# Optimization experiments

Measured on AMD Instinct MI355X. Metric: run time of the kernel, lower is better.

Reference implementation:

```python
import jax, jax.numpy as jnp
import numpy as np

B, S, D = 16, 4096, 128
LN_EPS = 1e-5
REC_EPS = 1e-8


def setup_inputs() -> dict:
    key = jax.random.key(0)
    k1, k2, k3, k4 = jax.random.split(key, 4)
    return {
        "C": jax.random.normal(k1, (B, S, D), dtype=jnp.float32),
        "V": jax.random.normal(k2, (B, S, D), dtype=jnp.float32),
        "W": jax.random.normal(k3, (B, S, D), dtype=jnp.float32),
        "encoder_context": jax.random.normal(k4, (B, D), dtype=jnp.float32),
        "time_modulation": jnp.full((1, 1, D), 0.5, dtype=jnp.float32),
        "context_modulation": jnp.full((1, D), 0.5, dtype=jnp.float32),
        "ln_weight": jnp.ones((D,), dtype=jnp.float32),
        "ln_bias": jnp.zeros((D,), dtype=jnp.float32),
    }


def reference(C, V, W, encoder_context, time_modulation, context_modulation, ln_weight, ln_bias):
    b_, s_, d_ = C.shape
    tm = time_modulation[0, 0]  # [D]
    # context gate is time-invariant: compute once
    ctx_add = jax.nn.sigmoid(encoder_context * context_modulation) * encoder_context  # [B,D]

    def step(carry, xs):
        a, bst = carry  # a: [B,1], bst: [B,D]
        c_t, v_t, w_t = xs  # each [B,D]
        decay = jax.nn.sigmoid(w_t * tm)  # [B,D]
        ec = jnp.exp(c_t)  # [B,D]
        a = decay.mean(axis=1, keepdims=True) * a + ec.sum(axis=1, keepdims=True)
        bst = decay * bst + ec * v_t + ctx_add
        out_t = bst / (a + REC_EPS)
        return (a, bst), out_t

    a0 = jnp.zeros((b_, 1), dtype=C.dtype)
    b0 = jnp.zeros((b_, d_), dtype=C.dtype)
    xs = (jnp.swapaxes(C, 0, 1), jnp.swapaxes(V, 0, 1), jnp.swapaxes(W, 0, 1))  # [S,B,D]
    _, ys = jax.lax.scan(step, (a0, b0), xs)  # ys: [S,B,D]
    res = jnp.swapaxes(ys, 0, 1)  # [B,S,D]

    mu = jnp.mean(res, axis=-1, keepdims=True)
    var = jnp.var(res, axis=-1, keepdims=True)
    normed = (res - mu) * jax.lax.rsqrt(var + LN_EPS)
    return normed * ln_weight + ln_bias
```

## Files before the change

kernel.cpp:

```cpp
#include <hip/hip_runtime.h>

#define BB   16
#define SS   4096
#define DD   128
#define NCH  256
#define TT   (SS / NCH)
#define GPB  4
#define NTHR 128

#define DT   16
#define SUBS 16
#define CPS  (NCH / SUBS)

#define LN_EPS  1e-5f
#define REC_EPS 1e-8f

__device__ __forceinline__ float fast_rcp(float x) { return __builtin_amdgcn_rcpf(x); }
__device__ __forceinline__ float sigm(float x) { return fast_rcp(1.0f + __expf(-x)); }

__device__ __forceinline__ unsigned pack_de(float d, float e) {
    unsigned ud = (__float_as_uint(d) + 0x8000u) >> 16;
    unsigned ue = (__float_as_uint(e) + 0x8000u) & 0xFFFF0000u;
    return ue | ud;
}
__device__ __forceinline__ float de_lo(unsigned u) { return __uint_as_float(u << 16); }
__device__ __forceinline__ float de_hi(unsigned u) { return __uint_as_float(u & 0xFFFF0000u); }

__device__ __forceinline__ void red2(float& a, float& b) {
#pragma unroll
    for (int m = 16; m >= 1; m >>= 1) {
        a += __shfl_xor(a, m, 64);
        b += __shfl_xor(b, m, 64);
    }
}

__global__ __launch_bounds__(NTHR) void pass1_kernel(
    const float* __restrict__ C, const float* __restrict__ V, const float* __restrict__ W,
    const float* __restrict__ enc, const float* __restrict__ tmod, const float* __restrict__ cmod,
    unsigned* __restrict__ DE,
    float* __restrict__ Pbuf, float* __restrict__ Qbuf,
    float* __restrict__ PaBuf, float* __restrict__ QaBuf,
    float* __restrict__ mbuf, float* __restrict__ ebuf)
{
    const int grp  = threadIdx.x >> 5;
    const int lane = threadIdx.x & 31;
    const int gc   = blockIdx.x * GPB + grp;
    const int b    = gc >> 8;
    const int ch   = gc & (NCH - 1);
    const int d4   = lane << 2;

    const float4 tm = *(const float4*)(tmod + d4);
    const float4 cm = *(const float4*)(cmod + d4);
    const float4 ec = *(const float4*)(enc + b * DD + d4);
    float4 ctx;
    ctx.x = sigm(ec.x * cm.x) * ec.x;
    ctx.y = sigm(ec.y * cm.y) * ec.y;
    ctx.z = sigm(ec.z * cm.z) * ec.z;
    ctx.w = sigm(ec.w * cm.w) * ec.w;

    float4 P = make_float4(1.f, 1.f, 1.f, 1.f);
    float4 Q = make_float4(0.f, 0.f, 0.f, 0.f);
    float pa = 1.f, qa = 0.f;

    const int t0 = ch * TT;
    const size_t base = ((size_t)b * SS + t0) * DD + d4;
    const float4* Cp = (const float4*)(C + base);
    const float4* Vp = (const float4*)(V + base);
    const float4* Wp = (const float4*)(W + base);
    uint4* DEp = (uint4*)(DE + base);

#pragma unroll 4
    for (int t = 0; t < TT; ++t) {
        const float4 c4 = Cp[t * (DD / 4)];
        const float4 v4 = Vp[t * (DD / 4)];
        const float4 w4 = Wp[t * (DD / 4)];
        float4 dec, e4;
        dec.x = sigm(w4.x * tm.x); dec.y = sigm(w4.y * tm.y);
        dec.z = sigm(w4.z * tm.z); dec.w = sigm(w4.w * tm.w);
        e4.x = __expf(c4.x); e4.y = __expf(c4.y);
        e4.z = __expf(c4.z); e4.w = __expf(c4.w);

        uint4 u;
        u.x = pack_de(dec.x, e4.x); u.y = pack_de(dec.y, e4.y);
        u.z = pack_de(dec.z, e4.z); u.w = pack_de(dec.w, e4.w);
        DEp[t * (DD / 4)] = u;

        Q.x = dec.x * Q.x + (e4.x * v4.x + ctx.x);
        Q.y = dec.y * Q.y + (e4.y * v4.y + ctx.y);
        Q.z = dec.z * Q.z + (e4.z * v4.z + ctx.z);
        Q.w = dec.w * Q.w + (e4.w * v4.w + ctx.w);
        P.x *= dec.x; P.y *= dec.y; P.z *= dec.z; P.w *= dec.w;

        float sd = (dec.x + dec.y) + (dec.z + dec.w);
        float se = (e4.x + e4.y) + (e4.z + e4.w);
        red2(sd, se);
        const float mt = sd * (1.0f / DD);
        pa *= mt;
        qa = mt * qa + se;
        if (lane == 0) {
            mbuf[(size_t)b * SS + t0 + t] = mt;
            ebuf[(size_t)b * SS + t0 + t] = se;
        }
    }

    *(float4*)(Pbuf + (size_t)gc * DD + d4) = P;
    *(float4*)(Qbuf + (size_t)gc * DD + d4) = Q;
    if (lane == 0) { PaBuf[gc] = pa; QaBuf[gc] = qa; }
}

__global__ __launch_bounds__(256) void pass2_kernel(
    const float* __restrict__ Pbuf, const float* __restrict__ Qbuf,
    const float* __restrict__ PaBuf, const float* __restrict__ QaBuf,
    float* __restrict__ bst0, float* __restrict__ a0)
{
    const int b   = blockIdx.x >> 3;
    const int dt  = blockIdx.x & 7;
    const int tid = threadIdx.x;
    const int dl  = tid & (DT - 1);
    const int sub = tid >> 4;
    const int d   = dt * DT + dl;

    __shared__ float cP[SUBS][DT], cQ[SUBS][DT], ent[SUBS][DT];
    __shared__ float sPa[NCH], sQa[NCH];

    const int ch0 = sub * CPS;
    const size_t base = ((size_t)b * NCH + ch0) * DD + d;
    float Pr[CPS], Qr[CPS];
    float p = 1.f, q = 0.f;
#pragma unroll
    for (int i = 0; i < CPS; ++i) {
        Pr[i] = Pbuf[base + (size_t)i * DD];
        Qr[i] = Qbuf[base + (size_t)i * DD];
        q = Pr[i] * q + Qr[i];
        p = Pr[i] * p;
    }
    cP[sub][dl] = p; cQ[sub][dl] = q;
    __syncthreads();

    if (tid < DT) {
        float s = 0.f;
#pragma unroll
        for (int sb = 0; sb < SUBS; ++sb) {
            ent[sb][tid] = s;
            s = cP[sb][tid] * s + cQ[sb][tid];
        }
    }
    __syncthreads();

    float s = ent[sub][dl];
#pragma unroll
    for (int i = 0; i < CPS; ++i) {
        bst0[base + (size_t)i * DD] = s;
        s = Pr[i] * s + Qr[i];
    }

    if (dt == 0) {
        float pa = PaBuf[b * NCH + tid];
        float qa = QaBuf[b * NCH + tid];
#pragma unroll
        for (int off = 1; off < NCH; off <<= 1) {
            sPa[tid] = pa; sQa[tid] = qa;
            __syncthreads();
            if (tid >= off) {
                const float pp = sPa[tid - off], qq = sQa[tid - off];
                qa = pa * qq + qa;
                pa = pa * pp;
            }
            __syncthreads();
        }
        sQa[tid] = qa;
        __syncthreads();
        a0[b * NCH + tid] = (tid == 0) ? 0.f : sQa[tid - 1];
    }
}

__global__ __launch_bounds__(NTHR) void pass3_kernel(
    const float* __restrict__ V, const unsigned* __restrict__ DE,
    const float* __restrict__ enc, const float* __restrict__ cmod,
    const float* __restrict__ lnw, const float* __restrict__ lnb,
    const float* __restrict__ bst0, const float* __restrict__ a0,
    const float* __restrict__ mbuf, const float* __restrict__ ebuf,
    float* __restrict__ out)
{
    const int grp  = threadIdx.x >> 5;
    const int lane = threadIdx.x & 31;
    const int gc   = blockIdx.x * GPB + grp;
    const int b    = gc >> 8;
    const int ch   = gc & (NCH - 1);
    const int d4   = lane << 2;

    const float4 cm = *(const float4*)(cmod + d4);
    const float4 ec = *(const float4*)(enc + b * DD + d4);
    float4 ctx;
    ctx.x = sigm(ec.x * cm.x) * ec.x;
    ctx.y = sigm(ec.y * cm.y) * ec.y;
    ctx.z = sigm(ec.z * cm.z) * ec.z;
    ctx.w = sigm(ec.w * cm.w) * ec.w;
    const float4 gw = *(const float4*)(lnw + d4);
    const float4 gb = *(const float4*)(lnb + d4);

    float4 bst = *(const float4*)(bst0 + (size_t)gc * DD + d4);
    float a = a0[gc];

    const int t0 = ch * TT;
    const size_t base = ((size_t)b * SS + t0) * DD + d4;
    const float4* Vp = (const float4*)(V + base);
    const uint4*  DEp = (const uint4*)(DE + base);
    float4* Op = (float4*)(out + base);
    const float* mp = mbuf + (size_t)b * SS + t0;
    const float* ep = ebuf + (size_t)b * SS + t0;

#pragma unroll 4
    for (int t = 0; t < TT; ++t) {
        const float4 v4 = Vp[t * (DD / 4)];
        const uint4  u  = DEp[t * (DD / 4)];
        const float mt = mp[t];
        const float et = ep[t];

        a = mt * a + et;
        bst.x = de_lo(u.x) * bst.x + (de_hi(u.x) * v4.x + ctx.x);
        bst.y = de_lo(u.y) * bst.y + (de_hi(u.y) * v4.y + ctx.y);
        bst.z = de_lo(u.z) * bst.z + (de_hi(u.z) * v4.z + ctx.z);
        bst.w = de_lo(u.w) * bst.w + (de_hi(u.w) * v4.w + ctx.w);

        const float inva = fast_rcp(a + REC_EPS);
        float4 o;
        o.x = bst.x * inva; o.y = bst.y * inva;
        o.z = bst.z * inva; o.w = bst.w * inva;

        float s1 = (o.x + o.y) + (o.z + o.w);
        float s2 = (o.x * o.x + o.y * o.y) + (o.z * o.z + o.w * o.w);
        red2(s1, s2);
        const float mu  = s1 * (1.0f / DD);
        const float var = s2 * (1.0f / DD) - mu * mu;
        const float rs  = rsqrtf(var + LN_EPS);

        float4 r;
        r.x = (o.x - mu) * rs * gw.x + gb.x;
        r.y = (o.y - mu) * rs * gw.y + gb.y;
        r.z = (o.z - mu) * rs * gw.z + gb.z;
        r.w = (o.w - mu) * rs * gw.w + gb.w;
        Op[t * (DD / 4)] = r;
    }
}

extern "C" void kernel_launch(void* const* d_in, const int* in_sizes, int n_in,
                              void* d_out, int out_size, void* d_ws, size_t ws_size,
                              hipStream_t stream)
{
    const float* C    = (const float*)d_in[0];
    const float* V    = (const float*)d_in[1];
    const float* W    = (const float*)d_in[2];
    const float* enc  = (const float*)d_in[3];
    const float* tmod = (const float*)d_in[4];
    const float* cmod = (const float*)d_in[5];
    const float* lnw  = (const float*)d_in[6];
    const float* lnb  = (const float*)d_in[7];
    float* out = (float*)d_out;

    float* ws    = (float*)d_ws;
    unsigned* DEbuf = (unsigned*)ws;
    float* Pbuf  = ws    + (size_t)BB * SS * DD;
    float* Qbuf  = Pbuf  + (size_t)BB * NCH * DD;
    float* bst0  = Qbuf  + (size_t)BB * NCH * DD;
    float* mbuf  = bst0  + (size_t)BB * NCH * DD;
    float* ebuf  = mbuf  + (size_t)BB * SS;
    float* PaBuf = ebuf  + (size_t)BB * SS;
    float* QaBuf = PaBuf + (size_t)BB * NCH;
    float* a0Buf = QaBuf + (size_t)BB * NCH;

    const int nblk = BB * NCH / GPB;
    pass1_kernel<<<nblk, NTHR, 0, stream>>>(C, V, W, enc, tmod, cmod, DEbuf,
                                            Pbuf, Qbuf, PaBuf, QaBuf, mbuf, ebuf);
    pass2_kernel<<<BB * 8, 256, 0, stream>>>(Pbuf, Qbuf, PaBuf, QaBuf, bst0, a0Buf);
    pass3_kernel<<<nblk, NTHR, 0, stream>>>(V, DEbuf, enc, cmod, lnw, lnb,
                                            bst0, a0Buf, mbuf, ebuf, out);
}
```

Measured before the change: 162.7 us.

## Map each chunk to a full 64-lane wave with DPP reductions

Pass 1 and pass 3 now give each sequential chunk a full 64-lane wavefront, with each lane handling two channels (float2) instead of four. Previously a chunk used 32 lanes handling float4. The cross-lane sums now use DPP row shifts plus a readlane instead of shfl_xor butterflies, and the per-step decay-mean and exp-sum scalars are merged into one float2 buffer. This doubles thread count and per-lane parallelism across the latency-bound recurrence and aims to cut reduction cost. In exchange, memory accesses become narrower 8-byte loads.

```diff
diff --git a/kernel.cpp b/kernel.cpp
--- a/kernel.cpp
+++ b/kernel.cpp
@@ -5,8 +5,8 @@
 #define DD   128
 #define NCH  256
 #define TT   (SS / NCH)
-#define GPB  4
-#define NTHR 128
+#define WPB  4
+#define NTHR 256
 
 #define DT   16
 #define SUBS 16
@@ -26,85 +26,84 @@
 __device__ __forceinline__ float de_lo(unsigned u) { return __uint_as_float(u << 16); }
 __device__ __forceinline__ float de_hi(unsigned u) { return __uint_as_float(u & 0xFFFF0000u); }
 
-__device__ __forceinline__ void red2(float& a, float& b) {
-#pragma unroll
-    for (int m = 16; m >= 1; m >>= 1) {
-        a += __shfl_xor(a, m, 64);
-        b += __shfl_xor(b, m, 64);
-    }
-}
-
-__global__ __launch_bounds__(NTHR) void pass1_kernel(
+template<int CTRL>
+__device__ __forceinline__ float dpp_mov0(float x) {
+    return __int_as_float(
+        __builtin_amdgcn_update_dpp(0, __float_as_int(x), CTRL, 0xF, 0xF, true));
+}
+
+__device__ __forceinline__ void wave_red2(float& a, float& b) {
+    a += dpp_mov0<0x111>(a); b += dpp_mov0<0x111>(b);
+    a += dpp_mov0<0x112>(a); b += dpp_mov0<0x112>(b);
+    a += dpp_mov0<0x114>(a); b += dpp_mov0<0x114>(b);
+    a += dpp_mov0<0x118>(a); b += dpp_mov0<0x118>(b);
+    a += dpp_mov0<0x142>(a); b += dpp_mov0<0x142>(b);
+    a += dpp_mov0<0x143>(a); b += dpp_mov0<0x143>(b);
+    a = __int_as_float(__builtin_amdgcn_readlane(__float_as_int(a), 63));
+    b = __int_as_float(__builtin_amdgcn_readlane(__float_as_int(b), 63));
+}
+
+__global__ __launch_bounds__(NTHR, 4) void pass1_kernel(
     const float* __restrict__ C, const float* __restrict__ V, const float* __restrict__ W,
     const float* __restrict__ enc, const float* __restrict__ tmod, const float* __restrict__ cmod,
     unsigned* __restrict__ DE,
     float* __restrict__ Pbuf, float* __restrict__ Qbuf,
     float* __restrict__ PaBuf, float* __restrict__ QaBuf,
-    float* __restrict__ mbuf, float* __restrict__ ebuf)
-{
-    const int grp  = threadIdx.x >> 5;
-    const int lane = threadIdx.x & 31;
-    const int gc   = blockIdx.x * GPB + grp;
+    float2* __restrict__ MEbuf)
+{
+    const int wv   = threadIdx.x >> 6;
+    const int lane = threadIdx.x & 63;
+    const int gc   = blockIdx.x * WPB + wv;
     const int b    = gc >> 8;
     const int ch   = gc & (NCH - 1);
-    const int d4   = lane << 2;
-
-    const float4 tm = *(const float4*)(tmod + d4);
-    const float4 cm = *(const float4*)(cmod + d4);
-    const float4 ec = *(const float4*)(enc + b * DD + d4);
-    float4 ctx;
+    const int d2   = lane << 1;
+
+    const float2 tm = *(const float2*)(tmod + d2);
+    const float2 cm = *(const float2*)(cmod + d2);
+    const float2 ec = *(const float2*)(enc + b * DD + d2);
+    float2 ctx;
     ctx.x = sigm(ec.x * cm.x) * ec.x;
     ctx.y = sigm(ec.y * cm.y) * ec.y;
-    ctx.z = sigm(ec.z * cm.z) * ec.z;
-    ctx.w = sigm(ec.w * cm.w) * ec.w;
-
-    float4 P = make_float4(1.f, 1.f, 1.f, 1.f);
-    float4 Q = make_float4(0.f, 0.f, 0.f, 0.f);
+
+    float2 P = make_float2(1.f, 1.f);
+    float2 Q = make_float2(0.f, 0.f);
     float pa = 1.f, qa = 0.f;
 
     const int t0 = ch * TT;
-    const size_t base = ((size_t)b * SS + t0) * DD + d4;
-    const float4* Cp = (const float4*)(C + base);
-    const float4* Vp = (const float4*)(V + base);
-    const float4* Wp = (const float4*)(W + base);
-    uint4* DEp = (uint4*)(DE + base);
+    const size_t base = ((size_t)b * SS + t0) * DD + d2;
+    const float2* Cp = (const float2*)(C + base);
+    const float2* Vp = (const float2*)(V + base);
+    const float2* Wp = (const float2*)(W + base);
+    uint2* DEp = (uint2*)(DE + base);
 
 #pragma unroll 4
     for (int t = 0; t < TT; ++t) {
-        const float4 c4 = Cp[t * (DD / 4)];
-        const float4 v4 = Vp[t * (DD / 4)];
-        const float4 w4 = Wp[t * (DD / 4)];
-        float4 dec, e4;
-        dec.x = sigm(w4.x * tm.x); dec.y = sigm(w4.y * tm.y);
-        dec.z = sigm(w4.z * tm.z); dec.w = sigm(w4.w * tm.w);
-        e4.x = __expf(c4.x); e4.y = __expf(c4.y);
-        e4.z = __expf(c4.z); e4.w = __expf(c4.w);
-
-        uint4 u;
-        u.x = pack_de(dec.x, e4.x); u.y = pack_de(dec.y, e4.y);
-        u.z = pack_de(dec.z, e4.z); u.w = pack_de(dec.w, e4.w);
-        DEp[t * (DD / 4)] = u;
-
-        Q.x = dec.x * Q.x + (e4.x * v4.x + ctx.x);
-        Q.y = dec.y * Q.y + (e4.y * v4.y + ctx.y);
-        Q.z = dec.z * Q.z + (e4.z * v4.z + ctx.z);
-        Q.w = dec.w * Q.w + (e4.w * v4.w + ctx.w);
-        P.x *= dec.x; P.y *= dec.y; P.z *= dec.z; P.w *= dec.w;
-
-        float sd = (dec.x + dec.y) + (dec.z + dec.w);
-        float se = (e4.x + e4.y) + (e4.z + e4.w);
-        red2(sd, se);
+        const float2 c2 = Cp[t * (DD / 2)];
+        const float2 v2 = Vp[t * (DD / 2)];
+        const float2 w2 = Wp[t * (DD / 2)];
+        float2 dec, e2;
+        dec.x = sigm(w2.x * tm.x); dec.y = sigm(w2.y * tm.y);
+        e2.x = __expf(c2.x); e2.y = __expf(c2.y);
+
+        uint2 u;
+        u.x = pack_de(dec.x, e2.x); u.y = pack_de(dec.y, e2.y);
+        DEp[t * (DD / 2)] = u;
+
+        Q.x = dec.x * Q.x + (e2.x * v2.x + ctx.x);
+        Q.y = dec.y * Q.y + (e2.y * v2.y + ctx.y);
+        P.x *= dec.x; P.y *= dec.y;
+
+        float sd = dec.x + dec.y;
+        float se = e2.x + e2.y;
+        wave_red2(sd, se);
         const float mt = sd * (1.0f / DD);
         pa *= mt;
         qa = mt * qa + se;
-        if (lane == 0) {
-            mbuf[(size_t)b * SS + t0 + t] = mt;
-            ebuf[(size_t)b * SS + t0 + t] = se;
-        }
-    }
-
-    *(float4*)(Pbuf + (size_t)gc * DD + d4) = P;
-    *(float4*)(Qbuf + (size_t)gc * DD + d4) = Q;
+        if (lane == 0) MEbuf[(size_t)b * SS + t0 + t] = make_float2(mt, se);
+    }
+
+    *(float2*)(Pbuf + (size_t)gc * DD + d2) = P;
+    *(float2*)(Qbuf + (size_t)gc * DD + d2) = Q;
     if (lane == 0) { PaBuf[gc] = pa; QaBuf[gc] = qa; }
 }
 
@@ -174,73 +173,64 @@
     }
 }
 
-__global__ __launch_bounds__(NTHR) void pass3_kernel(
+__global__ __launch_bounds__(NTHR, 4) void pass3_kernel(
     const float* __restrict__ V, const unsigned* __restrict__ DE,
     const float* __restrict__ enc, const float* __restrict__ cmod,
     const float* __restrict__ lnw, const float* __restrict__ lnb,
     const float* __restrict__ bst0, const float* __restrict__ a0,
-    const float* __restrict__ mbuf, const float* __restrict__ ebuf,
+    const float2* __restrict__ MEbuf,
     float* __restrict__ out)
 {
-    const int grp  = threadIdx.x >> 5;
-    const int lane = threadIdx.x & 31;
-    const int gc   = blockIdx.x * GPB + grp;
+    const int wv   = threadIdx.x >> 6;
+    const int lane = threadIdx.x & 63;
+    const int gc   = blockIdx.x * WPB + wv;
     const int b    = gc >> 8;
     const int ch   = gc & (NCH - 1);
-    const int d4   = lane << 2;
-
-    const float4 cm = *(const float4*)(cmod + d4);
-    const float4 ec = *(const float4*)(enc + b * DD + d4);
-    float4 ctx;
+    const int d2   = lane << 1;
+
+    const float2 cm = *(const float2*)(cmod + d2);
+    const float2 ec = *(const float2*)(enc + b * DD + d2);
+    float2 ctx;
     ctx.x = sigm(ec.x * cm.x) * ec.x;
     ctx.y = sigm(ec.y * cm.y) * ec.y;
-    ctx.z = sigm(ec.z * cm.z) * ec.z;
-    ctx.w = sigm(ec.w * cm.w) * ec.w;
-    const float4 gw = *(const float4*)(lnw + d4);
-    const float4 gb = *(const float4*)(lnb + d4);
-
-    float4 bst = *(const float4*)(bst0 + (size_t)gc * DD + d4);
+    const float2 gw = *(const float2*)(lnw + d2);
+    const float2 gb = *(const float2*)(lnb + d2);
+
+    float2 bst = *(const float2*)(bst0 + (size_t)gc * DD + d2);
     float a = a0[gc];
 
     const int t0 = ch * TT;
-    const size_t base = ((size_t)b * SS + t0) * DD + d4;
-    const float4* Vp = (const float4*)(V + base);
-    const uint4*  DEp = (const uint4*)(DE + base);
-    float4* Op = (float4*)(out + base);
-    const float* mp = mbuf + (size_t)b * SS + t0;
-    const float* ep = ebuf + (size_t)b * SS + t0;
+    const size_t base = ((size_t)b * SS + t0) * DD + d2;
+    const float2* Vp  = (const float2*)(V + base);
+    const uint2*  DEp = (const uint2*)(DE + base);
+    float2* Op = (float2*)(out + base);
+    const float2* MEp = MEbuf + (size_t)b * SS + t0;
 
 #pragma unroll 4
     for (int t = 0; t < TT; ++t) {
-        const float4 v4 = Vp[t * (DD / 4)];
-        const uint4  u  = DEp[t * (DD / 4)];
-        const float mt = mp[t];
-        const float et = ep[t];
-
-        a = mt * a + et;
-        bst.x = de_lo(u.x) * bst.x + (de_hi(u.x) * v4.x + ctx.x);
-        bst.y = de_lo(u.y) * bst.y + (de_hi(u.y) * v4.y + ctx.y);
-        bst.z = de_lo(u.z) * bst.z + (de_hi(u.z) * v4.z + ctx.z);
-        bst.w = de_lo(u.w) * bst.w + (de_hi(u.w) * v4.w + ctx.w);
+        const float2 v2 = Vp[t * (DD / 2)];
+        const uint2  u  = DEp[t * (DD / 2)];
+        const float2 me = MEp[t];
+
+        a = me.x * a + me.y;
+        bst.x = de_lo(u.x) * bst.x + (de_hi(u.x) * v2.x + ctx.x);
+        bst.y = de_lo(u.y) * bst.y + (de_hi(u.y) * v2.y + ctx.y);
 
         const float inva = fast_rcp(a + REC_EPS);
-        float4 o;
+        float2 o;
         o.x = bst.x * inva; o.y = bst.y * inva;
-        o.z = bst.z * inva; o.w = bst.w * inva;
-
-        float s1 = (o.x + o.y) + (o.z + o.w);
-        float s2 = (o.x * o.x + o.y * o.y) + (o.z * o.z + o.w * o.w);
-        red2(s1, s2);
+
+        float s1 = o.x + o.y;
+        float s2 = o.x * o.x + o.y * o.y;
+        wave_red2(s1, s2);
         const float mu  = s1 * (1.0f / DD);
         const float var = s2 * (1.0f / DD) - mu * mu;
         const float rs  = rsqrtf(var + LN_EPS);
 
-        float4 r;
+        float2 r;
         r.x = (o.x - mu) * rs * gw.x + gb.x;
         r.y = (o.y - mu) * rs * gw.y + gb.y;
-        r.z = (o.z - mu) * rs * gw.z + gb.z;
-        r.w = (o.w - mu) * rs * gw.w + gb.w;
-        Op[t * (DD / 4)] = r;
+        Op[t * (DD / 2)] = r;
     }
 }
 
@@ -263,16 +253,15 @@
     float* Pbuf  = ws    + (size_t)BB * SS * DD;
     float* Qbuf  = Pbuf  + (size_t)BB * NCH * DD;
     float* bst0  = Qbuf  + (size_t)BB * NCH * DD;
-    float* mbuf  = bst0  + (size_t)BB * NCH * DD;
-    float* ebuf  = mbuf  + (size_t)BB * SS;
-    float* PaBuf = ebuf  + (size_t)BB * SS;
+    float2* MEbuf = (float2*)(bst0 + (size_t)BB * NCH * DD);
+    float* PaBuf = (float*)(MEbuf + (size_t)BB * SS);
     float* QaBuf = PaBuf + (size_t)BB * NCH;
     float* a0Buf = QaBuf + (size_t)BB * NCH;
 
-    const int nblk = BB * NCH / GPB;
+    const int nblk = BB * NCH / WPB;
     pass1_kernel<<<nblk, NTHR, 0, stream>>>(C, V, W, enc, tmod, cmod, DEbuf,
-                                            Pbuf, Qbuf, PaBuf, QaBuf, mbuf, ebuf);
+                                            Pbuf, Qbuf, PaBuf, QaBuf, MEbuf);
     pass2_kernel<<<BB * 8, 256, 0, stream>>>(Pbuf, Qbuf, PaBuf, QaBuf, bst0, a0Buf);
     pass3_kernel<<<nblk, NTHR, 0, stream>>>(V, DEbuf, enc, cmod, lnw, lnb,
-                                            bst0, a0Buf, mbuf, ebuf, out);
-}
+                                            bst0, a0Buf, MEbuf, out);
+}
```

New measurement: 164.0 us. No clear change (+0.8%).
